# Optimization experiments

Measured on AMD Instinct MI355X. Metric: run time of the kernel, lower is better.

The kernel has to match this reference:

```python
import jax, jax.numpy as jnp
import numpy as np

NEG_SLOPE = 0.2  # PyG GATConv default leaky_relu slope

def gat_conv(x, src, dst, W, a_src, a_dst, bias, N):
    # Linear transform
    h = x @ W                      # [N, D]
    # Per-node attention logits (heads=1)
    al_src = h @ a_src             # [N]
    al_dst = h @ a_dst             # [N]
    e = jax.nn.leaky_relu(al_src[src] + al_dst[dst], NEG_SLOPE)  # [E]
    # Segment softmax over incoming edges of each destination node
    m = jax.ops.segment_max(e, dst, num_segments=N)
    ex = jnp.exp(e - m[dst])
    denom = jax.ops.segment_sum(ex, dst, num_segments=N)
    alpha = ex / denom[dst]        # [E]
    # Weighted scatter-aggregate of source features
    out = jax.ops.segment_sum(h[src] * alpha[:, None], dst, num_segments=N)
    return out + bias

def setup_inputs() -> dict:
    key = jax.random.key(0)
    ks = jax.random.split(key, 10)
    N, E, F_in, H, O = 50000, 800000, 128, 64, 64
    x = jax.random.normal(ks[0], (N, F_in), dtype=jnp.float32)
    edge_index = jax.random.randint(ks[1], (2, E), 0, N, dtype=jnp.int32)
    s = lambda k, shp, fan: jax.random.normal(k, shp, dtype=jnp.float32) / np.sqrt(fan)
    return {
        'x': x, 'edge_index': edge_index,
        'W1': s(ks[2], (F_in, H), F_in), 'a_src1': s(ks[3], (H,), H), 'a_dst1': s(ks[4], (H,), H), 'b1': jnp.zeros((H,), jnp.float32),
        'W2': s(ks[5], (H, O), H), 'a_src2': s(ks[6], (O,), O), 'a_dst2': s(ks[7], (O,), O), 'b2': jnp.zeros((O,), jnp.float32),
    }

def reference(x, edge_index, W1, a_src1, a_dst1, b1, W2, a_src2, a_dst2, b2):
    N = x.shape[0]
    loops = jnp.arange(N, dtype=edge_index.dtype)  # PyG adds self-loops by default
    src = jnp.concatenate([edge_index[0], loops])
    dst = jnp.concatenate([edge_index[1], loops])
    h = gat_conv(x, src, dst, W1, a_src1, a_dst1, b1, N)
    h = jax.nn.relu(h)
    # dropout(p=0.6) is identity in eval mode
    out = gat_conv(h, src, dst, W2, a_src2, a_dst2, b2, N)
    return out
```

## Files before the change

### kernel.cpp

```cpp
#include <hip/hip_runtime.h>
#include <hip/hip_bf16.h>

#define DEV static __device__ __forceinline__

typedef short bf16x8 __attribute__((ext_vector_type(8)));
typedef float f32x4  __attribute__((ext_vector_type(4)));
typedef unsigned u32x4 __attribute__((ext_vector_type(4)));

union U4 { uint4 u; bf16x8 s; };

DEV float b2f(__hip_bfloat16 v) { return __bfloat162float(v); }
DEV float lrelu(float e) { return e > 0.f ? e : 0.2f * e; }

DEV unsigned short f2bu(float f) {
    __hip_bfloat16 b = __float2bfloat16(f);
    return *reinterpret_cast<unsigned short*>(&b);
}
DEV float bu2f(unsigned short u) { return __uint_as_float((unsigned)u << 16); }

DEV float loadF(const void* p, size_t i, int f32) {
    if (f32) return ((const float*)p)[i];
    return b2f(((const __hip_bfloat16*)p)[i]);
}

DEV uint4 pack8(const unsigned short* t) {
    uint4 v;
    v.x = (unsigned)t[0] | ((unsigned)t[1] << 16);
    v.y = (unsigned)t[2] | ((unsigned)t[3] << 16);
    v.z = (unsigned)t[4] | ((unsigned)t[5] << 16);
    v.w = (unsigned)t[6] | ((unsigned)t[7] << 16);
    return v;
}

DEV u32x4 pack8v(const unsigned short* t) {
    u32x4 v;
    v.x = (unsigned)t[0] | ((unsigned)t[1] << 16);
    v.y = (unsigned)t[2] | ((unsigned)t[3] << 16);
    v.z = (unsigned)t[4] | ((unsigned)t[5] << 16);
    v.w = (unsigned)t[6] | ((unsigned)t[7] << 16);
    return v;
}

DEV void edge_sd(int i, int E, const int* __restrict__ src, const int* __restrict__ dst,
                 int& s, int& d) {
    if (i < E) { s = src[i]; d = dst[i]; }
    else       { s = d = i - E; }
}

DEV int detect_wave(const void* p, int n, int lane) {
    const unsigned short* u16 = (const unsigned short*)p;
    bool insane = false;
#pragma unroll
    for (int r = 0; r < 4; ++r) {
        int idx = lane + r * 64;
        if (idx < n) {
            unsigned short u = u16[idx];
            unsigned e = (u >> 7) & 0xFFu;
            insane |= (e >= 0xC8u) || (e == 0u && (u & 0x7Fu) != 0u);
        }
    }
    return (__ballot(insane) != 0ull) ? 1 : 0;
}

#define G_BIN 128

__global__ __launch_bounds__(256) void k_fused1(
    const void* __restrict__ x, const void* __restrict__ W,
    const void* __restrict__ a_s, const void* __restrict__ a_d,
    __hip_bfloat16* __restrict__ h, float* __restrict__ als, float* __restrict__ ald,
    int N, int gb, int nx, int nW1,
    const int* __restrict__ src, const int* __restrict__ dst,
    int* __restrict__ hist, int E, int EA, int chunk,
    const void* a5, int n5, const void* a6, int n6, const void* a7, int n7,
    const void* a8, int n8, const void* a9, int n9,
    int* __restrict__ flags)
{
    const int tid = threadIdx.x;
    const int bid = blockIdx.x;

    if (bid >= gb) {
        if (bid == gb + G_BIN) {
            const void* ps[9] = {x, W, a_s, a_d, a5, a6, a7, a8, a9};
            const int   ns[9] = {nx, nW1, 64, 64, n5, n6, n7, n8, n9};
            const int w = tid >> 6, lane = tid & 63;
            for (int k = w; k < 9; k += 4) {
                int f = detect_wave(ps[k], ns[k], lane);
                if (lane == 0) flags[k] = f;
            }
            return;
        }
        __shared__ int cnt[256];
        cnt[tid] = 0;
        __syncthreads();
        const int cb = bid - gb;
        const int lo = cb * chunk;
        const int hi = min(lo + chunk, EA);
        for (int i = lo + tid; i < hi; i += 256) {
            int s, d; edge_sd(i, E, src, dst, s, d);
            atomicAdd(&cnt[d >> 8], 1);
        }
        __syncthreads();
        hist[cb * 256 + tid] = cnt[tid];
        return;
    }

    __shared__ __align__(16) unsigned short sMem[2 * 64 * 136];
    __shared__ float sAs[64], sAd[64];
    __shared__ int sFl[4];
    unsigned short* sA = sMem;
    unsigned short* sB = sMem + 64 * 136;
    float* sOut = (float*)sMem;

    {
        const void* ps4[4] = {x, W, a_s, a_d};
        const int   ns4[4] = {nx, nW1, 64, 64};
        const int w = tid >> 6, lane = tid & 63;
        int f = detect_wave(ps4[w], ns4[w], lane);
        if (lane == 0) sFl[w] = f;
    }
    __syncthreads();
    const int fx = sFl[0], fw = sFl[1];

    const int row0 = bid * 64;
    if (tid < 64) sAs[tid] = loadF(a_s, tid, sFl[2]);
    else if (tid < 128) sAd[tid - 64] = loadF(a_d, tid - 64, sFl[3]);

    if (!fx) {
        const uint4* xg = (const uint4*)x;
#pragma unroll
        for (int it = 0; it < 2; ++it) {
            int g = tid + it * 256;
            int r = g >> 4, c16 = g & 15;
            uint4 v = (row0 + r < N) ? xg[(size_t)(row0 + r) * 16 + c16]
                                     : make_uint4(0, 0, 0, 0);
            *(uint4*)(sA + r * 136 + c16 * 8) = v;
        }
    } else {
        for (int i = tid; i < 64 * 128; i += 256) {
            int r = i >> 7, k = i & 127;
            float v = (row0 + r < N) ? ((const float*)x)[(size_t)(row0 + r) * 128 + k] : 0.f;
            sA[r * 136 + k] = f2bu(v);
        }
    }
    if (!fw) {
        const unsigned short* Wg = (const unsigned short*)W;
        const int n = tid & 63;
        int k0 = (tid >> 6) * 8;
#pragma unroll
        for (int rep = 0; rep < 4; ++rep, k0 += 32) {
            unsigned short t[8];
#pragma unroll
            for (int j = 0; j < 8; ++j) t[j] = Wg[(size_t)(k0 + j) * 64 + n];
            *(uint4*)(sB + n * 136 + k0) = pack8(t);
        }
    } else {
        const float* Wg = (const float*)W;
        for (int i = tid; i < 128 * 64; i += 256) {
            int k = i >> 6, n = i & 63;
            sB[n * 136 + k] = f2bu(Wg[i]);
        }
    }
    __syncthreads();

    const int w = tid >> 6, lane = tid & 63;
    const int m0 = w * 16;
    const int qr = lane >> 4;
    const int lc = lane & 15;

    bf16x8 afrag[4];
#pragma unroll
    for (int c = 0; c < 4; ++c) {
        U4 u; u.u = *(const uint4*)(sA + (m0 + lc) * 136 + c * 32 + qr * 8);
        afrag[c] = u.s;
    }
    f32x4 accs[4];
#pragma unroll
    for (int nt = 0; nt < 4; ++nt) {
        f32x4 acc = {0.f, 0.f, 0.f, 0.f};
#pragma unroll
        for (int c = 0; c < 4; ++c) {
            U4 u; u.u = *(const uint4*)(sB + (nt * 16 + lc) * 136 + c * 32 + qr * 8);
            acc = __builtin_amdgcn_mfma_f32_16x16x32_bf16(afrag[c], u.s, acc, 0, 0, 0);
        }
        accs[nt] = acc;
    }
    __syncthreads();

#pragma unroll
    for (int nt = 0; nt < 4; ++nt)
#pragma unroll
        for (int reg = 0; reg < 4; ++reg)
            sOut[(m0 + qr * 4 + reg) * 68 + nt * 16 + lc] = accs[nt][reg];
    __syncthreads();

    {
        const int r = tid >> 2, seg = tid & 3;
        const int row = row0 + r;
        const float* po = sOut + r * 68 + seg * 16;
        float ps = 0.f, pd = 0.f;
        unsigned short ob[16];
#pragma unroll
        for (int i = 0; i < 16; ++i) {
            float v = po[i];
            ps = fmaf(v, sAs[seg * 16 + i], ps);
            pd = fmaf(v, sAd[seg * 16 + i], pd);
            ob[i] = f2bu(v);
        }
        if (row < N) {
            uint4* hp = (uint4*)((unsigned short*)h + (size_t)row * 64 + seg * 16);
            hp[0] = pack8(ob);
            hp[1] = pack8(ob + 8);
        }
        ps += __shfl_xor(ps, 1, 64); ps += __shfl_xor(ps, 2, 64);
        pd += __shfl_xor(pd, 1, 64); pd += __shfl_xor(pd, 2, 64);
        if (seg == 0 && row < N) { als[row] = ps; ald[row] = pd; }
    }
}

__global__ __launch_bounds__(256) void k_binC2(
    const int* __restrict__ src, const int* __restrict__ dst,
    const int* __restrict__ hist, int* __restrict__ btot,
    unsigned* __restrict__ ebuf, int E, int EA, int chunk)
{
    __shared__ int sm[256];
    __shared__ int cur[256];
    const int tid = threadIdx.x;
    const int cb = blockIdx.x;

    int tot = 0, mine = 0;
#pragma unroll 4
    for (int c = 0; c < G_BIN; ++c) {
        int v = hist[c * 256 + tid];
        tot += v;
        if (c < cb) mine += v;
    }
    if (cb == 0) btot[tid] = tot;
    sm[tid] = tot;
    __syncthreads();
#pragma unroll
    for (int off = 1; off < 256; off <<= 1) {
        int t = (tid >= off) ? sm[tid - off] : 0;
        __syncthreads();
        sm[tid] += t;
        __syncthreads();
    }
    cur[tid] = (sm[tid] - tot) + mine;
    __syncthreads();
    const int lo = cb * chunk;
    const int hi = min(lo + chunk, EA);
    for (int i = lo + tid; i < hi; i += 256) {
        int s, d; edge_sd(i, E, src, dst, s, d);
        int pos = atomicAdd(&cur[d >> 8], 1);
        ebuf[pos] = ((unsigned)(d & 255) << 17) | (unsigned)s;
    }
}

__global__ __launch_bounds__(256) void k_binD(
    const unsigned* __restrict__ ebuf, const int* __restrict__ btot,
    const float* __restrict__ als,
    int* __restrict__ row_ptr, int2* __restrict__ ecol, int N)
{
    __shared__ int sm[256];
    __shared__ int cnt[256];
    __shared__ int pfx[256];
    const int tid = threadIdx.x;
    const int b = blockIdx.x;
    {
        int v = btot[tid];
        sm[tid] = v;
        __syncthreads();
#pragma unroll
        for (int off = 1; off < 256; off <<= 1) {
            int t = (tid >= off) ? sm[tid - off] : 0;
            __syncthreads();
            sm[tid] += t;
            __syncthreads();
        }
    }
    const int lo = (b == 0) ? 0 : sm[b - 1];
    const int hi = sm[b];
    cnt[tid] = 0;
    __syncthreads();
    for (int i = lo + tid; i < hi; i += 256)
        atomicAdd(&cnt[ebuf[i] >> 17], 1);
    __syncthreads();
    const int c = cnt[tid];
    pfx[tid] = c;
    __syncthreads();
#pragma unroll
    for (int off = 1; off < 256; off <<= 1) {
        int t = (tid >= off) ? pfx[tid - off] : 0;
        __syncthreads();
        pfx[tid] += t;
        __syncthreads();
    }
    const int excl = pfx[tid] - c;
    const int d = b * 256 + tid;
    if (d <= N) row_ptr[d] = lo + excl;
    __syncthreads();
    cnt[tid] = lo + excl;
    __syncthreads();
    for (int i = lo + tid; i < hi; i += 256) {
        unsigned v = ebuf[i];
        const int s = (int)(v & 0x1FFFFu);
        int pos = atomicAdd(&cnt[v >> 17], 1);
        ecol[pos] = make_int2(s, __float_as_int(als[s]));
    }
}

__global__ __launch_bounds__(256) void k_gemm2(
    __hip_bfloat16* __restrict__ agg, const void* __restrict__ b1,
    const void* __restrict__ W, const void* __restrict__ a_s,
    const void* __restrict__ a_d, const int* __restrict__ flags,
    float* __restrict__ als, float* __restrict__ ald, int N)
{
    __shared__ __align__(16) unsigned short sMem[2 * 64 * 72];
    __shared__ float sAs[64], sAd[64], sBias[64];
    unsigned short* sA = sMem;
    unsigned short* sB = sMem + 64 * 72;
    float* sOut = (float*)sMem;

    const int tid = threadIdx.x;
    const int row0 = blockIdx.x * 64;
    const int fw = flags[5];

    if (tid < 64) sAs[tid] = loadF(a_s, tid, flags[6]);
    else if (tid < 128) sAd[tid - 64] = loadF(a_d, tid - 64, flags[7]);
    else if (tid < 192) sBias[tid - 128] = loadF(b1, tid - 128, flags[4]);
    __syncthreads();

    {
        const uint4* ag = (const uint4*)agg;
#pragma unroll
        for (int it = 0; it < 2; ++it) {
            int g = tid + it * 256;
            int r = g >> 3, c8 = g & 7;
            uint4 v = (row0 + r < N) ? ag[(size_t)(row0 + r) * 8 + c8]
                                     : make_uint4(0, 0, 0, 0);
            unsigned short in[8] = {
                (unsigned short)(v.x & 0xFFFF), (unsigned short)(v.x >> 16),
                (unsigned short)(v.y & 0xFFFF), (unsigned short)(v.y >> 16),
                (unsigned short)(v.z & 0xFFFF), (unsigned short)(v.z >> 16),
                (unsigned short)(v.w & 0xFFFF), (unsigned short)(v.w >> 16)};
            unsigned short ob[8];
#pragma unroll
            for (int j = 0; j < 8; ++j) {
                float t = bu2f(in[j]) + sBias[c8 * 8 + j];
                ob[j] = f2bu(t > 0.f ? t : 0.f);
            }
            *(uint4*)(sA + r * 72 + c8 * 8) = pack8(ob);
        }
    }
    if (!fw) {
        const unsigned short* Wg = (const unsigned short*)W;
        const int n = tid & 63;
        int k0 = (tid >> 6) * 8;
#pragma unroll
        for (int rep = 0; rep < 2; ++rep, k0 += 32) {
            unsigned short t[8];
#pragma unroll
            for (int j = 0; j < 8; ++j) t[j] = Wg[(size_t)(k0 + j) * 64 + n];
            *(uint4*)(sB + n * 72 + k0) = pack8(t);
        }
    } else {
        const float* Wg = (const float*)W;
        for (int i = tid; i < 64 * 64; i += 256) {
            int k = i >> 6, n = i & 63;
            sB[n * 72 + k] = f2bu(Wg[i]);
        }
    }
    __syncthreads();

    const int w = tid >> 6, lane = tid & 63;
    const int m0 = w * 16;
    const int qr = lane >> 4, lc = lane & 15;

    bf16x8 afrag[2];
#pragma unroll
    for (int c = 0; c < 2; ++c) {
        U4 u; u.u = *(const uint4*)(sA + (m0 + lc) * 72 + c * 32 + qr * 8);
        afrag[c] = u.s;
    }
    f32x4 accs[4];
#pragma unroll
    for (int nt = 0; nt < 4; ++nt) {
        f32x4 acc = {0.f, 0.f, 0.f, 0.f};
#pragma unroll
        for (int c = 0; c < 2; ++c) {
            U4 u; u.u = *(const uint4*)(sB + (nt * 16 + lc) * 72 + c * 32 + qr * 8);
            acc = __builtin_amdgcn_mfma_f32_16x16x32_bf16(afrag[c], u.s, acc, 0, 0, 0);
        }
        accs[nt] = acc;
    }
    __syncthreads();
#pragma unroll
    for (int nt = 0; nt < 4; ++nt)
#pragma unroll
        for (int reg = 0; reg < 4; ++reg)
            sOut[(m0 + qr * 4 + reg) * 68 + nt * 16 + lc] = accs[nt][reg];
    __syncthreads();

    {
        const int r = tid >> 2, seg = tid & 3;
        const int row = row0 + r;
        const float* po = sOut + r * 68 + seg * 16;
        float ps = 0.f, pd = 0.f;
        unsigned short ob[16];
#pragma unroll
        for (int i = 0; i < 16; ++i) {
            float v = po[i];
            ps = fmaf(v, sAs[seg * 16 + i], ps);
            pd = fmaf(v, sAd[seg * 16 + i], pd);
            ob[i] = f2bu(v);
        }
        if (row < N) {
            uint4* hp = (uint4*)((unsigned short*)agg + (size_t)row * 64 + seg * 16);
            hp[0] = pack8(ob);
            hp[1] = pack8(ob + 8);
        }
        ps += __shfl_xor(ps, 1, 64); ps += __shfl_xor(ps, 2, 64);
        pd += __shfl_xor(pd, 1, 64); pd += __shfl_xor(pd, 2, 64);
        if (seg == 0 && row < N) { als[row] = ps; ald[row] = pd; }
    }
}

template<int MODE>
__global__ __launch_bounds__(256) void k_gather_t(
    const int* __restrict__ row_ptr, const int2* __restrict__ ecol,
    const float* __restrict__ als, const float* __restrict__ ald,
    const __hip_bfloat16* __restrict__ h,
    __hip_bfloat16* __restrict__ agg_out,
    void* __restrict__ final_out,
    const void* __restrict__ bias, const int* __restrict__ flags, int N)
{
    const int tid = threadIdx.x;
    const int lane = tid & 63;
    const int eg = lane >> 3, fg = lane & 7;
    const int wid = blockIdx.x * 4 + (tid >> 6);
    const int nw  = gridDim.x * 4;

    float bv[8]; int f0 = 0;
    if (MODE == 1) {
        f0 = flags[0];
#pragma unroll
        for (int k = 0; k < 8; ++k) bv[k] = loadF(bias, fg * 8 + k, flags[8]);
    }

    for (int d = wid; d < N; d += nw) {
        const float aldd = ald[d];
        const int beg = row_ptr[d], end = row_ptr[d + 1];
        float acc[8] = {0.f,0.f,0.f,0.f,0.f,0.f,0.f,0.f};
        float den = 0.f;
        int j = beg + eg;
        if (j < end) {
            int2 e = ecol[j];
            float aC = (MODE == 0) ? __int_as_float(e.y) : als[e.x];
            uint4 hvC = *reinterpret_cast<const uint4*>(h + (size_t)e.x * 64 + fg * 8);
            for (; j < end; j += 8) {
                const int jn = j + 8;
                int2 eN = make_int2(0, 0);
                float aN = 0.f;
                uint4 hvN = make_uint4(0, 0, 0, 0);
                if (jn < end) {
                    eN = ecol[jn];
                    aN = (MODE == 0) ? __int_as_float(eN.y) : als[eN.x];
                    hvN = *reinterpret_cast<const uint4*>(h + (size_t)eN.x * 64 + fg * 8);
                }
                const float w = __expf(lrelu(aC + aldd));
                den += w;
                acc[0] = fmaf(w, __uint_as_float(hvC.x << 16),          acc[0]);
                acc[1] = fmaf(w, __uint_as_float(hvC.x & 0xFFFF0000u),  acc[1]);
                acc[2] = fmaf(w, __uint_as_float(hvC.y << 16),          acc[2]);
                acc[3] = fmaf(w, __uint_as_float(hvC.y & 0xFFFF0000u),  acc[3]);
                acc[4] = fmaf(w, __uint_as_float(hvC.z << 16),          acc[4]);
                acc[5] = fmaf(w, __uint_as_float(hvC.z & 0xFFFF0000u),  acc[5]);
                acc[6] = fmaf(w, __uint_as_float(hvC.w << 16),          acc[6]);
                acc[7] = fmaf(w, __uint_as_float(hvC.w & 0xFFFF0000u),  acc[7]);
                e = eN; aC = aN; hvC = hvN;
            }
        }
#pragma unroll
        for (int off = 8; off <= 32; off <<= 1) {
            den += __shfl_xor(den, off, 64);
#pragma unroll
            for (int q = 0; q < 8; ++q) acc[q] += __shfl_xor(acc[q], off, 64);
        }
        if (eg == 0) {
            const float inv = 1.f / den;
            if (MODE == 1) {
                float vb[8];
#pragma unroll
                for (int q = 0; q < 8; ++q) vb[q] = fmaf(acc[q], inv, bv[q]);
                if (f0) {
                    float* o = (float*)final_out + (size_t)d * 64 + fg * 8;
                    f32x4 o0 = {vb[0], vb[1], vb[2], vb[3]};
                    f32x4 o1 = {vb[4], vb[5], vb[6], vb[7]};
                    __builtin_nontemporal_store(o0, (f32x4*)o);
                    __builtin_nontemporal_store(o1, (f32x4*)(o + 4));
                } else {
                    unsigned short ob[8];
#pragma unroll
                    for (int q = 0; q < 8; ++q) ob[q] = f2bu(vb[q]);
                    __builtin_nontemporal_store(pack8v(ob),
                        reinterpret_cast<u32x4*>((__hip_bfloat16*)final_out + (size_t)d * 64 + fg * 8));
                }
            } else {
                unsigned short ob[8];
#pragma unroll
                for (int q = 0; q < 8; ++q) ob[q] = f2bu(acc[q] * inv);
                __builtin_nontemporal_store(pack8v(ob),
                    reinterpret_cast<u32x4*>(agg_out + (size_t)d * 64 + fg * 8));
            }
        }
    }
}

extern "C" void kernel_launch(void* const* d_in, const int* in_sizes, int n_in,
                              void* d_out, int out_size, void* d_ws, size_t ws_size,
                              hipStream_t stream)
{
    const void* x   = d_in[0];
    const int*  ei  = (const int*)d_in[1];
    const void* W1  = d_in[2];
    const void* as1 = d_in[3];
    const void* ad1 = d_in[4];
    const void* b1  = d_in[5];
    const void* W2  = d_in[6];
    const void* as2 = d_in[7];
    const void* ad2 = d_in[8];
    const void* b2  = d_in[9];

    const int N  = in_sizes[0] / 128;
    const int E  = in_sizes[1] / 2;
    const int EA = E + N;
    const int* src = ei;
    const int* dst = ei + E;

    uintptr_t base = (uintptr_t)d_ws;
    auto alloc = [&](size_t bytes) { uintptr_t p = base; base += (bytes + 63) & ~(size_t)63; return p; };
    int*      flags    = (int*)alloc(64 * 4);
    float*    als      = (float*)alloc((size_t)N * 4);
    float*    ald      = (float*)alloc((size_t)N * 4);
    int*      row_ptr  = (int*)alloc((size_t)(N + 1) * 4);
    int*      hist     = (int*)alloc((size_t)G_BIN * 256 * 4);
    int*      btot     = (int*)alloc(256 * 4);
    unsigned* ebuf     = (unsigned*)alloc((size_t)EA * 4);
    int2*     ecol     = (int2*)alloc((size_t)EA * 8);
    __hip_bfloat16* hbuf   = (__hip_bfloat16*)alloc((size_t)N * 64 * 2);
    __hip_bfloat16* aggbuf = (__hip_bfloat16*)alloc((size_t)N * 64 * 2);

    const int gatherb = 2048;
    const int gb  = (N + 63) / 64;
    const int NBK = (N + 255) / 256;
    const int chunk = (EA + G_BIN - 1) / G_BIN;

    k_fused1<<<gb + G_BIN + 1, 256, 0, stream>>>(
        x, W1, as1, ad1, hbuf, als, ald, N, gb, in_sizes[0], in_sizes[2],
        src, dst, hist, E, EA, chunk,
        b1, in_sizes[5], W2, in_sizes[6], as2, in_sizes[7], ad2, in_sizes[8],
        b2, in_sizes[9], flags);
    k_binC2<<<G_BIN, 256, 0, stream>>>(src, dst, hist, btot, ebuf, E, EA, chunk);
    k_binD<<<NBK, 256, 0, stream>>>(ebuf, btot, als, row_ptr, ecol, N);

    k_gather_t<0><<<gatherb, 256, 0, stream>>>(row_ptr, ecol, nullptr, ald, hbuf,
                                               aggbuf, nullptr, nullptr, flags, N);
    k_gemm2<<<gb, 256, 0, stream>>>(aggbuf, b1, W2, as2, ad2, flags, als, ald, N);
    k_gather_t<1><<<gatherb, 256, 0, stream>>>(row_ptr, ecol, als, ald, aggbuf,
                                               nullptr, d_out, b2, flags, N);
    (void)out_size; (void)ws_size; (void)n_in;
}
```

Before: 200.8 us.

## Fuse layer-1 gather with layer-2 GEMM and attention logits in one kernel

The layer-1 edge-gather kernel and the separate layer-2 GEMM kernel are merged. Each block aggregates up to 28 destination nodes into an LDS tile, applies bias and ReLU, then multiplies that tile by W2 with MFMA. It also computes the layer-2 source and destination logits and writes h2 directly. This removes one launch and the global write and re-read of the intermediate aggregation buffer. In exchange, every block reloads W2 into LDS, and the block-wide barriers between the gather and the GEMM may reduce latency hiding in the memory-bound gather.

```diff
diff --git a/kernel.cpp b/kernel.cpp
--- a/kernel.cpp
+++ b/kernel.cpp
@@ -308,51 +308,26 @@
     }
 }
 
-__global__ __launch_bounds__(256) void k_gemm2(
-    __hip_bfloat16* __restrict__ agg, const void* __restrict__ b1,
-    const void* __restrict__ W, const void* __restrict__ a_s,
-    const void* __restrict__ a_d, const int* __restrict__ flags,
-    float* __restrict__ als, float* __restrict__ ald, int N)
+__global__ __launch_bounds__(256) void k_gat1g2(
+    const int* __restrict__ row_ptr, const int2* __restrict__ ecol,
+    const float* __restrict__ ald,
+    const __hip_bfloat16* __restrict__ h,
+    __hip_bfloat16* __restrict__ h2,
+    float* __restrict__ als2, float* __restrict__ ald2,
+    const void* __restrict__ b1, const void* __restrict__ W2,
+    const void* __restrict__ a_s2, const void* __restrict__ a_d2,
+    const int* __restrict__ flags, int N, int npw)
 {
-    __shared__ __align__(16) unsigned short sMem[2 * 64 * 72];
-    __shared__ float sAs[64], sAd[64], sBias[64];
-    unsigned short* sA = sMem;
-    unsigned short* sB = sMem + 64 * 72;
-    float* sOut = (float*)sMem;
+    __shared__ __align__(16) unsigned short sB[64 * 72];
+    __shared__ __align__(16) unsigned short sRel[32 * 72];
+    __shared__ float sB1[64], sAs2[64], sAd2[64];
+    __shared__ float sPs[32], sPd[32];
+    __shared__ int sNode[32];
 
     const int tid = threadIdx.x;
-    const int row0 = blockIdx.x * 64;
-    const int fw = flags[5];
-
-    if (tid < 64) sAs[tid] = loadF(a_s, tid, flags[6]);
-    else if (tid < 128) sAd[tid - 64] = loadF(a_d, tid - 64, flags[7]);
-    else if (tid < 192) sBias[tid - 128] = loadF(b1, tid - 128, flags[4]);
-    __syncthreads();
-
-    {
-        const uint4* ag = (const uint4*)agg;
-#pragma unroll
-        for (int it = 0; it < 2; ++it) {
-            int g = tid + it * 256;
-            int r = g >> 3, c8 = g & 7;
-            uint4 v = (row0 + r < N) ? ag[(size_t)(row0 + r) * 8 + c8]
-                                     : make_uint4(0, 0, 0, 0);
-            unsigned short in[8] = {
-                (unsigned short)(v.x & 0xFFFF), (unsigned short)(v.x >> 16),
-                (unsigned short)(v.y & 0xFFFF), (unsigned short)(v.y >> 16),
-                (unsigned short)(v.z & 0xFFFF), (unsigned short)(v.z >> 16),
-                (unsigned short)(v.w & 0xFFFF), (unsigned short)(v.w >> 16)};
-            unsigned short ob[8];
-#pragma unroll
-            for (int j = 0; j < 8; ++j) {
-                float t = bu2f(in[j]) + sBias[c8 * 8 + j];
-                ob[j] = f2bu(t > 0.f ? t : 0.f);
-            }
-            *(uint4*)(sA + r * 72 + c8 * 8) = pack8(ob);
-        }
-    }
-    if (!fw) {
-        const unsigned short* Wg = (const unsigned short*)W;
+
+    if (!flags[5]) {
+        const unsigned short* Wg = (const unsigned short*)W2;
         const int n = tid & 63;
         int k0 = (tid >> 6) * 8;
 #pragma unroll
@@ -363,90 +338,29 @@
             *(uint4*)(sB + n * 72 + k0) = pack8(t);
         }
     } else {
-        const float* Wg = (const float*)W;
+        const float* Wg = (const float*)W2;
         for (int i = tid; i < 64 * 64; i += 256) {
             int k = i >> 6, n = i & 63;
             sB[n * 72 + k] = f2bu(Wg[i]);
         }
     }
-    __syncthreads();
-
-    const int w = tid >> 6, lane = tid & 63;
-    const int m0 = w * 16;
-    const int qr = lane >> 4, lc = lane & 15;
-
-    bf16x8 afrag[2];
-#pragma unroll
-    for (int c = 0; c < 2; ++c) {
-        U4 u; u.u = *(const uint4*)(sA + (m0 + lc) * 72 + c * 32 + qr * 8);
-        afrag[c] = u.s;
-    }
-    f32x4 accs[4];
-#pragma unroll
-    for (int nt = 0; nt < 4; ++nt) {
-        f32x4 acc = {0.f, 0.f, 0.f, 0.f};
-#pragma unroll
-        for (int c = 0; c < 2; ++c) {
-            U4 u; u.u = *(const uint4*)(sB + (nt * 16 + lc) * 72 + c * 32 + qr * 8);
-            acc = __builtin_amdgcn_mfma_f32_16x16x32_bf16(afrag[c], u.s, acc, 0, 0, 0);
-        }
-        accs[nt] = acc;
-    }
-    __syncthreads();
-#pragma unroll
-    for (int nt = 0; nt < 4; ++nt)
-#pragma unroll
-        for (int reg = 0; reg < 4; ++reg)
-            sOut[(m0 + qr * 4 + reg) * 68 + nt * 16 + lc] = accs[nt][reg];
-    __syncthreads();
-
-    {
-        const int r = tid >> 2, seg = tid & 3;
-        const int row = row0 + r;
-        const float* po = sOut + r * 68 + seg * 16;
-        float ps = 0.f, pd = 0.f;
-        unsigned short ob[16];
-#pragma unroll
-        for (int i = 0; i < 16; ++i) {
-            float v = po[i];
-            ps = fmaf(v, sAs[seg * 16 + i], ps);
-            pd = fmaf(v, sAd[seg * 16 + i], pd);
-            ob[i] = f2bu(v);
-        }
-        if (row < N) {
-            uint4* hp = (uint4*)((unsigned short*)agg + (size_t)row * 64 + seg * 16);
-            hp[0] = pack8(ob);
-            hp[1] = pack8(ob + 8);
-        }
-        ps += __shfl_xor(ps, 1, 64); ps += __shfl_xor(ps, 2, 64);
-        pd += __shfl_xor(pd, 1, 64); pd += __shfl_xor(pd, 2, 64);
-        if (seg == 0 && row < N) { als[row] = ps; ald[row] = pd; }
-    }
-}
-
-template<int MODE>
-__global__ __launch_bounds__(256) void k_gather_t(
-    const int* __restrict__ row_ptr, const int2* __restrict__ ecol,
-    const float* __restrict__ als, const float* __restrict__ ald,
-    const __hip_bfloat16* __restrict__ h,
-    __hip_bfloat16* __restrict__ agg_out,
-    void* __restrict__ final_out,
-    const void* __restrict__ bias, const int* __restrict__ flags, int N)
-{
-    const int tid = threadIdx.x;
-    const int lane = tid & 63;
+    if (tid < 64) sB1[tid] = loadF(b1, tid, flags[4]);
+    else if (tid < 128) sAs2[tid - 64] = loadF(a_s2, tid - 64, flags[6]);
+    else if (tid < 192) sAd2[tid - 128] = loadF(a_d2, tid - 128, flags[7]);
+    if (tid < 32) { sNode[tid] = -1; sPs[tid] = 0.f; sPd[tid] = 0.f; }
+    for (int i = tid; i < 32 * 72; i += 256) sRel[i] = 0;
+    __syncthreads();
+
+    const int lane = tid & 63, wave = tid >> 6;
     const int eg = lane >> 3, fg = lane & 7;
-    const int wid = blockIdx.x * 4 + (tid >> 6);
+    const int wid = blockIdx.x * 4 + wave;
     const int nw  = gridDim.x * 4;
 
-    float bv[8]; int f0 = 0;
-    if (MODE == 1) {
-        f0 = flags[0];
-#pragma unroll
-        for (int k = 0; k < 8; ++k) bv[k] = loadF(bias, fg * 8 + k, flags[8]);
-    }
-
-    for (int d = wid; d < N; d += nw) {
+    for (int k = 0; k < npw; ++k) {
+        const int d = wid + k * nw;
+        if (d >= N) break;
+        const int slot = wave * npw + k;
+        if (lane == 0) sNode[slot] = d;
         const float aldd = ald[d];
         const int beg = row_ptr[d], end = row_ptr[d + 1];
         float acc[8] = {0.f,0.f,0.f,0.f,0.f,0.f,0.f,0.f};
@@ -454,16 +368,14 @@
         int j = beg + eg;
         if (j < end) {
             int2 e = ecol[j];
-            float aC = (MODE == 0) ? __int_as_float(e.y) : als[e.x];
+            float aC = __int_as_float(e.y);
             uint4 hvC = *reinterpret_cast<const uint4*>(h + (size_t)e.x * 64 + fg * 8);
             for (; j < end; j += 8) {
                 const int jn = j + 8;
                 int2 eN = make_int2(0, 0);
-                float aN = 0.f;
                 uint4 hvN = make_uint4(0, 0, 0, 0);
                 if (jn < end) {
                     eN = ecol[jn];
-                    aN = (MODE == 0) ? __int_as_float(eN.y) : als[eN.x];
                     hvN = *reinterpret_cast<const uint4*>(h + (size_t)eN.x * 64 + fg * 8);
                 }
                 const float w = __expf(lrelu(aC + aldd));
@@ -476,7 +388,7 @@
                 acc[5] = fmaf(w, __uint_as_float(hvC.z & 0xFFFF0000u),  acc[5]);
                 acc[6] = fmaf(w, __uint_as_float(hvC.w << 16),          acc[6]);
                 acc[7] = fmaf(w, __uint_as_float(hvC.w & 0xFFFF0000u),  acc[7]);
-                e = eN; aC = aN; hvC = hvN;
+                aC = __int_as_float(eN.y); hvC = hvN;
             }
         }
 #pragma unroll
@@ -487,29 +399,158 @@
         }
         if (eg == 0) {
             const float inv = 1.f / den;
-            if (MODE == 1) {
-                float vb[8];
-#pragma unroll
-                for (int q = 0; q < 8; ++q) vb[q] = fmaf(acc[q], inv, bv[q]);
-                if (f0) {
-                    float* o = (float*)final_out + (size_t)d * 64 + fg * 8;
-                    f32x4 o0 = {vb[0], vb[1], vb[2], vb[3]};
-                    f32x4 o1 = {vb[4], vb[5], vb[6], vb[7]};
-                    __builtin_nontemporal_store(o0, (f32x4*)o);
-                    __builtin_nontemporal_store(o1, (f32x4*)(o + 4));
-                } else {
-                    unsigned short ob[8];
-#pragma unroll
-                    for (int q = 0; q < 8; ++q) ob[q] = f2bu(vb[q]);
-                    __builtin_nontemporal_store(pack8v(ob),
-                        reinterpret_cast<u32x4*>((__hip_bfloat16*)final_out + (size_t)d * 64 + fg * 8));
+            unsigned short ob[8];
+#pragma unroll
+            for (int q = 0; q < 8; ++q) {
+                float v = fmaf(acc[q], inv, sB1[fg * 8 + q]);
+                ob[q] = f2bu(v > 0.f ? v : 0.f);
+            }
+            *(uint4*)(sRel + slot * 72 + fg * 8) = pack8(ob);
+        }
+    }
+    __syncthreads();
+
+    {
+        const int qr = lane >> 4, lc = lane & 15;
+        const int roww = wave & 1, colpair = wave >> 1;
+        const int m0 = roww * 16;
+
+        bf16x8 af[2];
+#pragma unroll
+        for (int c = 0; c < 2; ++c) {
+            U4 u; u.u = *(const uint4*)(sRel + (m0 + lc) * 72 + c * 32 + qr * 8);
+            af[c] = u.s;
+        }
+        __syncthreads();
+
+        f32x4 accs[2];
+#pragma unroll
+        for (int t = 0; t < 2; ++t) {
+            const int ct = colpair * 2 + t;
+            f32x4 acc = {0.f, 0.f, 0.f, 0.f};
+#pragma unroll
+            for (int c = 0; c < 2; ++c) {
+                U4 u; u.u = *(const uint4*)(sB + (ct * 16 + lc) * 72 + c * 32 + qr * 8);
+                acc = __builtin_amdgcn_mfma_f32_16x16x32_bf16(af[c], u.s, acc, 0, 0, 0);
+            }
+            accs[t] = acc;
+        }
+
+        float psr[4] = {0.f,0.f,0.f,0.f}, pdr[4] = {0.f,0.f,0.f,0.f};
+#pragma unroll
+        for (int t = 0; t < 2; ++t) {
+            const int col = (colpair * 2 + t) * 16 + lc;
+            const float cs = sAs2[col], cd = sAd2[col];
+#pragma unroll
+            for (int reg = 0; reg < 4; ++reg) {
+                psr[reg] = fmaf(accs[t][reg], cs, psr[reg]);
+                pdr[reg] = fmaf(accs[t][reg], cd, pdr[reg]);
+                sRel[(m0 + qr * 4 + reg) * 72 + col] = f2bu(accs[t][reg]);
+            }
+        }
+#pragma unroll
+        for (int off = 1; off <= 8; off <<= 1) {
+#pragma unroll
+            for (int reg = 0; reg < 4; ++reg) {
+                psr[reg] += __shfl_xor(psr[reg], off, 64);
+                pdr[reg] += __shfl_xor(pdr[reg], off, 64);
+            }
+        }
+        if (lc == 0) {
+#pragma unroll
+            for (int reg = 0; reg < 4; ++reg) {
+                atomicAdd(&sPs[m0 + qr * 4 + reg], psr[reg]);
+                atomicAdd(&sPd[m0 + qr * 4 + reg], pdr[reg]);
+            }
+        }
+    }
+    __syncthreads();
+
+    {
+        const int r = tid >> 3, seg = tid & 7;
+        const int d = sNode[r];
+        if (d >= 0) {
+            uint4 v = *(const uint4*)(sRel + r * 72 + seg * 8);
+            *(uint4*)((unsigned short*)h2 + (size_t)d * 64 + seg * 8) = v;
+            if (seg == 0) { als2[d] = sPs[r]; ald2[d] = sPd[r]; }
+        }
+    }
+}
+
+__global__ __launch_bounds__(256) void k_gather2(
+    const int* __restrict__ row_ptr, const int2* __restrict__ ecol,
+    const float* __restrict__ als, const float* __restrict__ ald,
+    const __hip_bfloat16* __restrict__ h,
+    void* __restrict__ final_out,
+    const void* __restrict__ bias, const int* __restrict__ flags, int N)
+{
+    const int tid = threadIdx.x;
+    const int lane = tid & 63;
+    const int eg = lane >> 3, fg = lane & 7;
+    const int wid = blockIdx.x * 4 + (tid >> 6);
+    const int nw  = gridDim.x * 4;
+
+    float bv[8];
+    const int f0 = flags[0];
+#pragma unroll
+    for (int k = 0; k < 8; ++k) bv[k] = loadF(bias, fg * 8 + k, flags[8]);
+
+    for (int d = wid; d < N; d += nw) {
+        const float aldd = ald[d];
+        const int beg = row_ptr[d], end = row_ptr[d + 1];
+        float acc[8] = {0.f,0.f,0.f,0.f,0.f,0.f,0.f,0.f};
+        float den = 0.f;
+        int j = beg + eg;
+        if (j < end) {
+            int2 e = ecol[j];
+            float aC = als[e.x];
+            uint4 hvC = *reinterpret_cast<const uint4*>(h + (size_t)e.x * 64 + fg * 8);
+            for (; j < end; j += 8) {
+                const int jn = j + 8;
+                int2 eN = make_int2(0, 0);
+                float aN = 0.f;
+                uint4 hvN = make_uint4(0, 0, 0, 0);
+                if (jn < end) {
+                    eN = ecol[jn];
+                    aN = als[eN.x];
+                    hvN = *reinterpret_cast<const uint4*>(h + (size_t)eN.x * 64 + fg * 8);
                 }
+                const float w = __expf(lrelu(aC + aldd));
+                den += w;
+                acc[0] = fmaf(w, __uint_as_float(hvC.x << 16),          acc[0]);
+                acc[1] = fmaf(w, __uint_as_float(hvC.x & 0xFFFF0000u),  acc[1]);
+                acc[2] = fmaf(w, __uint_as_float(hvC.y << 16),          acc[2]);
+                acc[3] = fmaf(w, __uint_as_float(hvC.y & 0xFFFF0000u),  acc[3]);
+                acc[4] = fmaf(w, __uint_as_float(hvC.z << 16),          acc[4]);
+                acc[5] = fmaf(w, __uint_as_float(hvC.z & 0xFFFF0000u),  acc[5]);
+                acc[6] = fmaf(w, __uint_as_float(hvC.w << 16),          acc[6]);
+                acc[7] = fmaf(w, __uint_as_float(hvC.w & 0xFFFF0000u),  acc[7]);
+                aC = aN; hvC = hvN;
+            }
+        }
+#pragma unroll
+        for (int off = 8; off <= 32; off <<= 1) {
+            den += __shfl_xor(den, off, 64);
+#pragma unroll
+            for (int q = 0; q < 8; ++q) acc[q] += __shfl_xor(acc[q], off, 64);
+        }
+        if (eg == 0) {
+            const float inv = 1.f / den;
+            float vb[8];
+#pragma unroll
+            for (int q = 0; q < 8; ++q) vb[q] = fmaf(acc[q], inv, bv[q]);
+            if (f0) {
+                float* o = (float*)final_out + (size_t)d * 64 + fg * 8;
+                f32x4 o0 = {vb[0], vb[1], vb[2], vb[3]};
+                f32x4 o1 = {vb[4], vb[5], vb[6], vb[7]};
+                __builtin_nontemporal_store(o0, (f32x4*)o);
+                __builtin_nontemporal_store(o1, (f32x4*)(o + 4));
             } else {
                 unsigned short ob[8];
 #pragma unroll
-                for (int q = 0; q < 8; ++q) ob[q] = f2bu(acc[q] * inv);
+                for (int q = 0; q < 8; ++q) ob[q] = f2bu(vb[q]);
                 __builtin_nontemporal_store(pack8v(ob),
-                    reinterpret_cast<u32x4*>(agg_out + (size_t)d * 64 + fg * 8));
+                    reinterpret_cast<u32x4*>((__hip_bfloat16*)final_out + (size_t)d * 64 + fg * 8));
             }
         }
     }
@@ -541,15 +582,18 @@
     int*      flags    = (int*)alloc(64 * 4);
     float*    als      = (float*)alloc((size_t)N * 4);
     float*    ald      = (float*)alloc((size_t)N * 4);
+    float*    als2     = (float*)alloc((size_t)N * 4);
+    float*    ald2     = (float*)alloc((size_t)N * 4);
     int*      row_ptr  = (int*)alloc((size_t)(N + 1) * 4);
     int*      hist     = (int*)alloc((size_t)G_BIN * 256 * 4);
     int*      btot     = (int*)alloc(256 * 4);
     unsigned* ebuf     = (unsigned*)alloc((size_t)EA * 4);
     int2*     ecol     = (int2*)alloc((size_t)EA * 8);
     __hip_bfloat16* hbuf   = (__hip_bfloat16*)alloc((size_t)N * 64 * 2);
-    __hip_bfloat16* aggbuf = (__hip_bfloat16*)alloc((size_t)N * 64 * 2);
+    __hip_bfloat16* h2buf  = (__hip_bfloat16*)alloc((size_t)N * 64 * 2);
 
     const int gatherb = 2048;
+    const int npw = (N + gatherb * 4 - 1) / (gatherb * 4);
     const int gb  = (N + 63) / 64;
     const int NBK = (N + 255) / 256;
     const int chunk = (EA + G_BIN - 1) / G_BIN;
@@ -562,10 +606,10 @@
     k_binC2<<<G_BIN, 256, 0, stream>>>(src, dst, hist, btot, ebuf, E, EA, chunk);
     k_binD<<<NBK, 256, 0, stream>>>(ebuf, btot, als, row_ptr, ecol, N);
 
-    k_gather_t<0><<<gatherb, 256, 0, stream>>>(row_ptr, ecol, nullptr, ald, hbuf,
-                                               aggbuf, nullptr, nullptr, flags, N);
-    k_gemm2<<<gb, 256, 0, stream>>>(aggbuf, b1, W2, as2, ad2, flags, als, ald, N);
-    k_gather_t<1><<<gatherb, 256, 0, stream>>>(row_ptr, ecol, als, ald, aggbuf,
-                                               nullptr, d_out, b2, flags, N);
+    k_gat1g2<<<gatherb, 256, 0, stream>>>(row_ptr, ecol, ald, hbuf, h2buf,
+                                          als2, ald2, b1, W2, as2, ad2,
+                                          flags, N, npw);
+    k_gather2<<<gatherb, 256, 0, stream>>>(row_ptr, ecol, als2, ald2, h2buf,
+                                           d_out, b2, flags, N);
     (void)out_size; (void)ws_size; (void)n_in;
 }
```

Result: no change. 202.7 us (+0.9%).

## Fold edge scatter into histogram blocks and drop separate binning kernel

Applied to the files above, without the earlier changes.

The histogram blocks in the first fused kernel now also scan their local counts and scatter edges into a per-chunk local bucket layout in ebuf, removing the separate k_binC2 launch. The final binning kernel rebuilds global bucket offsets from the per-chunk histograms and uses a binary search over chunk prefix sums to locate each bucket's edges, which are now scattered across chunks. This removes one kernel launch and one full pass over src/dst, at the cost of extra per-element search and less contiguous reads in the CSR-building kernel. It also drops a dead `e = eN` assignment in the gather loop.

```diff
diff --git a/kernel.cpp b/kernel.cpp
--- a/kernel.cpp
+++ b/kernel.cpp
@@ -70,7 +70,8 @@
     __hip_bfloat16* __restrict__ h, float* __restrict__ als, float* __restrict__ ald,
     int N, int gb, int nx, int nW1,
     const int* __restrict__ src, const int* __restrict__ dst,
-    int* __restrict__ hist, int E, int EA, int chunk,
+    int* __restrict__ hist, int* __restrict__ histScan,
+    unsigned* __restrict__ ebuf, int E, int EA, int chunk,
     const void* a5, int n5, const void* a6, int n6, const void* a7, int n7,
     const void* a8, int n8, const void* a9, int n9,
     int* __restrict__ flags)
@@ -89,18 +90,36 @@
             }
             return;
         }
-        __shared__ int cnt[256];
-        cnt[tid] = 0;
+        __shared__ int cntA[256], smA[256], curA[256];
+        cntA[tid] = 0;
         __syncthreads();
         const int cb = bid - gb;
         const int lo = cb * chunk;
         const int hi = min(lo + chunk, EA);
         for (int i = lo + tid; i < hi; i += 256) {
             int s, d; edge_sd(i, E, src, dst, s, d);
-            atomicAdd(&cnt[d >> 8], 1);
-        }
-        __syncthreads();
-        hist[cb * 256 + tid] = cnt[tid];
+            atomicAdd(&cntA[d >> 8], 1);
+        }
+        __syncthreads();
+        hist[cb * 256 + tid] = cntA[tid];
+        smA[tid] = cntA[tid];
+        __syncthreads();
+#pragma unroll
+        for (int off = 1; off < 256; off <<= 1) {
+            int t = (tid >= off) ? smA[tid - off] : 0;
+            __syncthreads();
+            smA[tid] += t;
+            __syncthreads();
+        }
+        const int excl = smA[tid] - cntA[tid];
+        histScan[cb * 256 + tid] = excl;
+        curA[tid] = lo + excl;
+        __syncthreads();
+        for (int i = lo + tid; i < hi; i += 256) {
+            int s, d; edge_sd(i, E, src, dst, s, d);
+            int pos = atomicAdd(&curA[d >> 8], 1);
+            ebuf[pos] = ((unsigned)(d & 255) << 17) | (unsigned)s;
+        }
         return;
     }
 
@@ -217,72 +236,54 @@
     }
 }
 
-__global__ __launch_bounds__(256) void k_binC2(
-    const int* __restrict__ src, const int* __restrict__ dst,
-    const int* __restrict__ hist, int* __restrict__ btot,
-    unsigned* __restrict__ ebuf, int E, int EA, int chunk)
+__global__ __launch_bounds__(256) void k_binD2(
+    const unsigned* __restrict__ ebuf, const int* __restrict__ hist,
+    const int* __restrict__ histScan, const float* __restrict__ als,
+    int* __restrict__ row_ptr, int2* __restrict__ ecol, int N, int chunk)
 {
-    __shared__ int sm[256];
-    __shared__ int cur[256];
-    const int tid = threadIdx.x;
-    const int cb = blockIdx.x;
-
-    int tot = 0, mine = 0;
-#pragma unroll 4
-    for (int c = 0; c < G_BIN; ++c) {
-        int v = hist[c * 256 + tid];
-        tot += v;
-        if (c < cb) mine += v;
-    }
-    if (cb == 0) btot[tid] = tot;
-    sm[tid] = tot;
-    __syncthreads();
-#pragma unroll
-    for (int off = 1; off < 256; off <<= 1) {
-        int t = (tid >= off) ? sm[tid - off] : 0;
-        __syncthreads();
-        sm[tid] += t;
-        __syncthreads();
-    }
-    cur[tid] = (sm[tid] - tot) + mine;
-    __syncthreads();
-    const int lo = cb * chunk;
-    const int hi = min(lo + chunk, EA);
-    for (int i = lo + tid; i < hi; i += 256) {
-        int s, d; edge_sd(i, E, src, dst, s, d);
-        int pos = atomicAdd(&cur[d >> 8], 1);
-        ebuf[pos] = ((unsigned)(d & 255) << 17) | (unsigned)s;
-    }
-}
-
-__global__ __launch_bounds__(256) void k_binD(
-    const unsigned* __restrict__ ebuf, const int* __restrict__ btot,
-    const float* __restrict__ als,
-    int* __restrict__ row_ptr, int2* __restrict__ ecol, int N)
-{
-    __shared__ int sm[256];
-    __shared__ int cnt[256];
-    __shared__ int pfx[256];
+    __shared__ int sTot[256];
+    __shared__ int rStart[G_BIN], rPfx[G_BIN];
+    __shared__ int cnt[256], pfx[256];
     const int tid = threadIdx.x;
     const int b = blockIdx.x;
-    {
-        int v = btot[tid];
-        sm[tid] = v;
-        __syncthreads();
-#pragma unroll
-        for (int off = 1; off < 256; off <<= 1) {
-            int t = (tid >= off) ? sm[tid - off] : 0;
-            __syncthreads();
-            sm[tid] += t;
-            __syncthreads();
-        }
-    }
-    const int lo = (b == 0) ? 0 : sm[b - 1];
-    const int hi = sm[b];
+
+    int tot = 0;
+#pragma unroll 4
+    for (int cb = 0; cb < G_BIN; ++cb) tot += hist[cb * 256 + tid];
+    sTot[tid] = tot;
+    __syncthreads();
+#pragma unroll
+    for (int off = 1; off < 256; off <<= 1) {
+        int t = (tid >= off) ? sTot[tid - off] : 0;
+        __syncthreads();
+        sTot[tid] += t;
+        __syncthreads();
+    }
+    const int lo = (b == 0) ? 0 : sTot[b - 1];
+    const int m  = sTot[b] - lo;
+
+    if (tid < G_BIN) {
+        rStart[tid] = tid * chunk + histScan[tid * 256 + b];
+        rPfx[tid]   = hist[tid * 256 + b];
+    }
+    __syncthreads();
+#pragma unroll
+    for (int off = 1; off < G_BIN; off <<= 1) {
+        int t = (tid < G_BIN && tid >= off) ? rPfx[tid - off] : 0;
+        __syncthreads();
+        if (tid < G_BIN) rPfx[tid] += t;
+        __syncthreads();
+    }
+
     cnt[tid] = 0;
     __syncthreads();
-    for (int i = lo + tid; i < hi; i += 256)
-        atomicAdd(&cnt[ebuf[i] >> 17], 1);
+    for (int i = tid; i < m; i += 256) {
+        int loS = 0, hiS = G_BIN - 1;
+        while (loS < hiS) { int mid = (loS + hiS) >> 1; if (rPfx[mid] > i) hiS = mid; else loS = mid + 1; }
+        const int off = i - (loS ? rPfx[loS - 1] : 0);
+        unsigned v = ebuf[rStart[loS] + off];
+        atomicAdd(&cnt[v >> 17], 1);
+    }
     __syncthreads();
     const int c = cnt[tid];
     pfx[tid] = c;
@@ -300,8 +301,12 @@
     __syncthreads();
     cnt[tid] = lo + excl;
     __syncthreads();
-    for (int i = lo + tid; i < hi; i += 256) {
-        unsigned v = ebuf[i];
+
+    for (int i = tid; i < m; i += 256) {
+        int loS = 0, hiS = G_BIN - 1;
+        while (loS < hiS) { int mid = (loS + hiS) >> 1; if (rPfx[mid] > i) hiS = mid; else loS = mid + 1; }
+        const int off = i - (loS ? rPfx[loS - 1] : 0);
+        unsigned v = ebuf[rStart[loS] + off];
         const int s = (int)(v & 0x1FFFFu);
         int pos = atomicAdd(&cnt[v >> 17], 1);
         ecol[pos] = make_int2(s, __float_as_int(als[s]));
@@ -476,7 +481,7 @@
                 acc[5] = fmaf(w, __uint_as_float(hvC.z & 0xFFFF0000u),  acc[5]);
                 acc[6] = fmaf(w, __uint_as_float(hvC.w << 16),          acc[6]);
                 acc[7] = fmaf(w, __uint_as_float(hvC.w & 0xFFFF0000u),  acc[7]);
-                e = eN; aC = aN; hvC = hvN;
+                aC = aN; hvC = hvN;
             }
         }
 #pragma unroll
@@ -536,6 +541,8 @@
     const int* src = ei;
     const int* dst = ei + E;
 
+    const int chunk = (EA + G_BIN - 1) / G_BIN;
+
     uintptr_t base = (uintptr_t)d_ws;
     auto alloc = [&](size_t bytes) { uintptr_t p = base; base += (bytes + 63) & ~(size_t)63; return p; };
     int*      flags    = (int*)alloc(64 * 4);
@@ -543,8 +550,8 @@
     float*    ald      = (float*)alloc((size_t)N * 4);
     int*      row_ptr  = (int*)alloc((size_t)(N + 1) * 4);
     int*      hist     = (int*)alloc((size_t)G_BIN * 256 * 4);
-    int*      btot     = (int*)alloc(256 * 4);
-    unsigned* ebuf     = (unsigned*)alloc((size_t)EA * 4);
+    int*      histScan = (int*)alloc((size_t)G_BIN * 256 * 4);
+    unsigned* ebuf     = (unsigned*)alloc((size_t)G_BIN * chunk * 4);
     int2*     ecol     = (int2*)alloc((size_t)EA * 8);
     __hip_bfloat16* hbuf   = (__hip_bfloat16*)alloc((size_t)N * 64 * 2);
     __hip_bfloat16* aggbuf = (__hip_bfloat16*)alloc((size_t)N * 64 * 2);
@@ -552,15 +559,13 @@
     const int gatherb = 2048;
     const int gb  = (N + 63) / 64;
     const int NBK = (N + 255) / 256;
-    const int chunk = (EA + G_BIN - 1) / G_BIN;
 
     k_fused1<<<gb + G_BIN + 1, 256, 0, stream>>>(
         x, W1, as1, ad1, hbuf, als, ald, N, gb, in_sizes[0], in_sizes[2],
-        src, dst, hist, E, EA, chunk,
+        src, dst, hist, histScan, ebuf, E, EA, chunk,
         b1, in_sizes[5], W2, in_sizes[6], as2, in_sizes[7], ad2, in_sizes[8],
         b2, in_sizes[9], flags);
-    k_binC2<<<G_BIN, 256, 0, stream>>>(src, dst, hist, btot, ebuf, E, EA, chunk);
-    k_binD<<<NBK, 256, 0, stream>>>(ebuf, btot, als, row_ptr, ecol, N);
+    k_binD2<<<NBK, 256, 0, stream>>>(ebuf, hist, histScan, als, row_ptr, ecol, N, chunk);
 
     k_gather_t<0><<<gatherb, 256, 0, stream>>>(row_ptr, ecol, nullptr, ald, hbuf,
                                                aggbuf, nullptr, nullptr, flags, N);
```

Result: slower. 205.4 us (+2.3%).
